# Optimization experiments

Measured on AMD Instinct MI355X. Metric: run time of the kernel, lower is better.

## Reference

```python
import jax, jax.numpy as jnp
import numpy as np

H = 128; F = 64; G = 50; L = 4; CUT = 10.0
M = 256; K = 8; A = 32
N_TOPO = M * A; N = M * K * A; NCONF = M * K
E_CONF = N * 16; E_GRAPH = N_TOPO * 4
ATOM_TYPES = 100; BOND_TYPES = 10
OFFSETS = jnp.linspace(0.0, CUT, G)
GCOEFF = -0.5 / (CUT / (G - 1)) ** 2  # GaussianSmearing coeff
BN_EPS = 1e-5


def batchnorm(x, g, b):
    # BatchNorm1d in training mode: batch statistics over nodes
    mu = x.mean(0)
    var = ((x - mu) ** 2).mean(0)
    return (x - mu) * jax.lax.rsqrt(var + BN_EPS) * g + b


def setup_inputs():
    key = jax.random.key(0)
    ks = jax.random.split(key, 20)
    s = lambda k, shp: (jax.random.normal(k, shp) * 0.05).astype(jnp.float32)
    inp = {}
    inp["x_topo"] = jax.random.randint(ks[0], (N_TOPO,), 0, ATOM_TYPES)
    inp["pos"] = jax.random.normal(ks[1], (N, 3), dtype=jnp.float32) * 3.0
    inp["edge_index_conf"] = jax.random.randint(ks[2], (2, E_CONF), 0, N)
    inp["edge_index_graph"] = jax.random.randint(ks[3], (2, E_GRAPH), 0, N_TOPO)
    inp["edge_attr_graph"] = jax.random.randint(ks[4], (E_GRAPH,), 0, BOND_TYPES)
    # conf_node_batch: for molecule i, repeat arange(A)+i*A over K conformers
    cnb = (np.arange(M)[:, None, None] * A + np.broadcast_to(np.arange(A), (K, A))).reshape(-1)
    inp["conf_node_batch"] = jnp.asarray(cnb, dtype=jnp.int32)
    inp["pos_batch"] = jnp.repeat(jnp.arange(NCONF), A).astype(jnp.int32)
    inp["conf_batch"] = jnp.repeat(jnp.arange(M), K).astype(jnp.int32)
    # parameters
    inp["atom_emb"] = s(ks[5], (ATOM_TYPES, H))
    inp["cf_lin1_w"] = s(ks[6], (L, H, F))
    inp["cf_mlp_w1"] = s(ks[7], (L, G, F)); inp["cf_mlp_b1"] = jnp.zeros((L, F), jnp.float32)
    inp["cf_mlp_w2"] = s(ks[8], (L, F, F)); inp["cf_mlp_b2"] = jnp.zeros((L, F), jnp.float32)
    inp["cf_lin2_w"] = s(ks[9], (L, F, H)); inp["cf_lin2_b"] = jnp.zeros((L, H), jnp.float32)
    inp["lin_w"] = s(ks[10], (L, H, H)); inp["lin_b"] = jnp.zeros((L, H), jnp.float32)
    inp["bond_emb"] = s(ks[11], (L, BOND_TYPES, H))
    inp["gin_w1"] = s(ks[12], (L, H, H)); inp["gin_b1"] = jnp.zeros((L, H), jnp.float32)
    inp["gin_w2"] = s(ks[13], (L, H, H)); inp["gin_b2"] = jnp.zeros((L, H), jnp.float32)
    inp["gin_bn_g"] = jnp.ones((L, H), jnp.float32); inp["gin_bn_b"] = jnp.zeros((L, H), jnp.float32)
    inp["bn_g"] = jnp.ones((L, H), jnp.float32); inp["bn_b"] = jnp.zeros((L, H), jnp.float32)
    inp["gin_eps"] = jnp.zeros((L,), jnp.float32)
    inp["out_w1"] = s(ks[14], (H, H)); inp["out_b1"] = jnp.zeros((H,), jnp.float32)
    inp["out_w2"] = s(ks[15], (H, 1)); inp["out_b2"] = jnp.zeros((1,), jnp.float32)
    return inp


def _forward(x_topo, edge_index_conf, edge_index_graph, edge_attr_graph,
             conf_node_batch, pos_batch, conf_batch,
             pos, atom_emb, cf_lin1_w, cf_mlp_w1, cf_mlp_b1, cf_mlp_w2, cf_mlp_b2,
             cf_lin2_w, cf_lin2_b, lin_w, lin_b, bond_emb,
             gin_w1, gin_b1, gin_w2, gin_b2, gin_bn_g, gin_bn_b, bn_g, bn_b,
             gin_eps, out_w1, out_b1, out_w2, out_b2):
    # AtomEncoder on topo graph, broadcast to all conformers
    x = atom_emb[x_topo][conf_node_batch]                      # [N, H]
    row, col = edge_index_conf[0], edge_index_conf[1]
    d = pos[row] - pos[col]
    ew = jnp.sqrt(jnp.sum(d * d, axis=-1) + 1e-12)             # edge_weight_conf [E_conf]
    ea = jnp.exp(GCOEFF * (ew[:, None] - OFFSETS) ** 2)        # GaussianSmearing [E_conf, G]
    cwin = 0.5 * (jnp.cos(ew * jnp.pi / CUT) + 1.0)            # SchNet cosine cutoff
    gr, gc = edge_index_graph[0], edge_index_graph[1]
    for l in range(L):
        # CFConv branch (use_conf)
        Wf = (jax.nn.relu(ea @ cf_mlp_w1[l] + cf_mlp_b1[l]) @ cf_mlp_w2[l] + cf_mlp_b2[l]) * cwin[:, None]
        h = x @ cf_lin1_w[l]                                   # lin1, no bias
        agg = jax.ops.segment_sum(h[row] * Wf, col, num_segments=N)
        h = agg @ cf_lin2_w[l] + cf_lin2_b[l]                  # lin2
        h = jax.nn.relu(h)
        h = h @ lin_w[l] + lin_b[l]
        out = x + h                                            # residual
        # GIN branch on topo graph (use_graph)
        x_agg = jax.ops.segment_max(x, conf_node_batch, num_segments=N_TOPO)
        eemb = bond_emb[l][edge_attr_graph]                    # BondEncoder
        magg = jax.ops.segment_sum(jax.nn.relu(x_agg[gr] + eemb), gc, num_segments=N_TOPO)
        hg = (1.0 + gin_eps[l]) * x_agg + magg
        hg = jax.nn.relu(batchnorm(hg @ gin_w1[l] + gin_b1[l], gin_bn_g[l], gin_bn_b[l]))
        hg = hg @ gin_w2[l] + gin_b2[l]
        hg = batchnorm(hg, bn_g[l], bn_b[l])
        out = out + hg[conf_node_batch]
        x = jax.nn.relu(out)
    x = jax.ops.segment_max(x, pos_batch, num_segments=NCONF)  # pool atoms -> conformers
    x = jax.ops.segment_max(x, conf_batch, num_segments=M)     # pool conformers -> molecules
    x = jax.nn.relu(x @ out_w1 + out_b1) @ out_w2 + out_b2     # out_layer
    return x                                                   # training mode: no clamp


def reference(x_topo, pos, edge_index_conf, edge_index_graph, edge_attr_graph,
              conf_node_batch, pos_batch, conf_batch,
              atom_emb, cf_lin1_w, cf_mlp_w1, cf_mlp_b1, cf_mlp_w2, cf_mlp_b2,
              cf_lin2_w, cf_lin2_b, lin_w, lin_b, bond_emb,
              gin_w1, gin_b1, gin_w2, gin_b2, gin_bn_g, gin_bn_b, bn_g, bn_b,
              gin_eps, out_w1, out_b1, out_w2, out_b2):
    return _forward(x_topo, edge_index_conf, edge_index_graph, edge_attr_graph,
                    conf_node_batch, pos_batch, conf_batch,
                    pos, atom_emb, cf_lin1_w, cf_mlp_w1, cf_mlp_b1, cf_mlp_w2, cf_mlp_b2,
                    cf_lin2_w, cf_lin2_b, lin_w, lin_b, bond_emb,
                    gin_w1, gin_b1, gin_w2, gin_b2, gin_bn_g, gin_bn_b, bn_g, bn_b,
                    gin_eps, out_w1, out_b1, out_w2, out_b2)
```

## Files before the change

kernel.cpp:

```cpp
#include <hip/hip_runtime.h>
#include <hip/hip_bf16.h>

#define EC 1048576
#define NN 65536
#define NT 8192
#define MM 256
#define HH 128
#define FF 64
#define GG 50
#define EG 32768

#define TBL 2048
#define TBL_SHIFT 11
#define TRANGE 14.0f

#define CAP 32
#define OVF_CAP 8192
#define NEB (NN * 64 / 256)
#define SEB (8 * (EC / 256))

constexpr float STEP = 10.0f / 49.0f;
constexpr float GC = -0.5f / (STEP * STEP);

typedef __attribute__((ext_vector_type(8))) short bf16x8;
typedef __attribute__((ext_vector_type(4))) float f32x4;

__device__ __forceinline__ ushort f2b(float v) {
    __hip_bfloat16 h = __float2bfloat16(v);
    return *(ushort*)&h;
}
__device__ __forceinline__ float b2f(ushort u) {
    return __uint_as_float(((unsigned)u) << 16);
}

__global__ __launch_bounds__(256) void setup_kernel(
    const int* __restrict__ eic, const int* __restrict__ cnb,
    const int* __restrict__ eig, const float* __restrict__ pos,
    const float* __restrict__ emb, const int* __restrict__ xtopo,
    int* __restrict__ degC, ushort* __restrict__ uu16, ushort* __restrict__ xb)
{
    int b = blockIdx.x, tid = threadIdx.x;
    if (b < EC / 256) {
        int e = b * 256 + tid;
        int r = eic[e], c = eic[EC + e];
        float dx = pos[r*3+0] - pos[c*3+0];
        float dy = pos[r*3+1] - pos[c*3+1];
        float dz = pos[r*3+2] - pos[c*3+2];
        float w = sqrtf(dx*dx + dy*dy + dz*dz + 1e-12f);
        float u = fminf(w * ((TBL - 1) / TRANGE), 2046.96875f);
        uu16[e] = (ushort)(int)(u * 32.0f);
    } else if (b < EC / 256 + EG / 256) {
        atomicAdd(&degC[eig[EG + (b - EC / 256) * 256 + tid]], 1);
    } else {
        int idx = (b - EC / 256 - EG / 256) * 256 + tid;
        int n = idx >> 4;
        int f8 = (idx & 15) << 3;
        const float* e = emb + (size_t)xtopo[cnb[n]] * HH + f8;
        float4 v0 = *(const float4*)e;
        float4 v1 = *(const float4*)(e + 4);
        ushort u[8] = {f2b(v0.x), f2b(v0.y), f2b(v0.z), f2b(v0.w),
                       f2b(v1.x), f2b(v1.y), f2b(v1.z), f2b(v1.w)};
        *(bf16x8*)(xb + ((size_t)idx << 3)) = *(const bf16x8*)u;
    }
}

__global__ __launch_bounds__(256) void scanC_kernel(
    const int* __restrict__ degC, int* __restrict__ offsC, int* __restrict__ curC)
{
    __shared__ int s[256];
    __shared__ int base;
    int tid = threadIdx.x;
    if (tid == 0) base = 0;
    __syncthreads();
    for (int c = 0; c < NT / 256; c++) {
        int v = degC[c * 256 + tid];
        s[tid] = v;
        __syncthreads();
        for (int off = 1; off < 256; off <<= 1) {
            int t = (tid >= off) ? s[tid - off] : 0;
            __syncthreads();
            s[tid] += t;
            __syncthreads();
        }
        int excl = s[tid] - v + base;
        offsC[c * 256 + tid] = excl;
        curC[c * 256 + tid] = excl;
        __syncthreads();
        if (tid == 255) base += s[255];
        __syncthreads();
    }
    if (tid == 0) offsC[NT] = EG;
}

__global__ __launch_bounds__(256) void scatter_all_kernel(
    const int* __restrict__ eic, const ushort* __restrict__ uu16,
    const int* __restrict__ eig, const int* __restrict__ eattr,
    int* __restrict__ cntA, int* __restrict__ curC,
    int* __restrict__ pay_pad, int2* __restrict__ gpay,
    int* __restrict__ ovf_cnt, int2* __restrict__ ovf)
{
    int b = blockIdx.x, tid = threadIdx.x;
    if (b < SEB) {
        int part = b & 7;
        int e = (b >> 3) * 256 + tid;
        int c = eic[EC + e];
        if ((c >> 13) != part) return;
        int pay = ((int)uu16[e] << 16) | (eic[e] & 0xFFFF);
        int slot = atomicAdd(&cntA[c], 1);
        if (slot < CAP) {
            pay_pad[c * CAP + slot] = pay;
        } else {
            int o = atomicAdd(ovf_cnt, 1);
            if (o < OVF_CAP) ovf[o] = make_int2(c, pay);
        }
    } else {
        int e = (b - SEB) * 256 + tid;
        int p = atomicAdd(&curC[eig[EG + e]], 1);
        gpay[p] = make_int2(eig[e], eattr[e]);
    }
}

__global__ __launch_bounds__(64) void build_table_kernel(
    const float* __restrict__ w1a, const float* __restrict__ b1a,
    const float* __restrict__ w2a, const float* __restrict__ b2a,
    float* __restrict__ table_all)
{
    int l = blockIdx.x >> TBL_SHIFT;
    int p = blockIdx.x & (TBL - 1);
    int lane = threadIdx.x;
    const float* w1 = w1a + (size_t)l * GG * FF;
    const float* b1 = b1a + (size_t)l * FF;
    const float* w2 = w2a + (size_t)l * FF * FF;
    const float* b2 = b2a + (size_t)l * FF;
    float w = p * (TRANGE / (TBL - 1));
    float t = b1[lane];
    for (int g = 0; g < GG; g++) {
        float d = w - g * STEP;
        float ea = __expf(GC * d * d);
        t = fmaf(ea, w1[g * 64 + lane], t);
    }
    __shared__ float ts[64];
    ts[lane] = fmaxf(t, 0.f);
    __syncthreads();
    float wf = b2[lane];
    for (int i = 0; i < 64; i++)
        wf = fmaf(ts[i], w2[i * 64 + lane], wf);
    float cw = 0.5f * (__cosf(w * (3.14159265358979323846f / 10.0f)) + 1.0f);
    table_all[((size_t)l * TBL + p) * 64 + lane] = wf * cw;
}

__global__ __launch_bounds__(256) void pack_table_kernel(
    const float* __restrict__ table_all, ushort2* __restrict__ table2_all)
{
    int idx = blockIdx.x * 256 + threadIdx.x;
    int f = idx & 63;
    int rest = idx >> 6;
    int i = rest & (TBL - 1);
    int l = rest >> TBL_SHIFT;
    const float* T = table_all + ((size_t)l * TBL) * 64;
    float t0 = T[(size_t)i * 64 + f];
    float t1 = (i + 1 < TBL) ? T[(size_t)(i + 1) * 64 + f] : 0.f;
    table2_all[idx] = make_ushort2(f2b(t0), f2b(t1 - t0));
}

__device__ __forceinline__ void prep_one(
    const float* __restrict__ W, ushort* __restrict__ Wf, int K, int N, int idx)
{
    int sz = K * N;
    int l = idx / sz;
    int t = idx - l * sz;
    int j = t & 7;
    int lane = (t >> 3) & 63;
    int rest = t >> 9;
    int KTl = K >> 5;
    int kt = rest % KTl;
    int nt = rest / KTl;
    int k = kt * 32 + (lane >> 4) * 8 + j;
    int n = nt * 16 + (lane & 15);
    Wf[idx] = f2b(W[(size_t)l * sz + (size_t)k * N + n]);
}

__global__ __launch_bounds__(256) void prep_all_kernel(
    const float* __restrict__ cf_lin1_w, const float* __restrict__ cf_lin2_w,
    const float* __restrict__ lin_w, const float* __restrict__ gin_w1,
    const float* __restrict__ gin_w2,
    ushort* __restrict__ w1f, ushort* __restrict__ w2f, ushort* __restrict__ wlf,
    ushort* __restrict__ gw1f, ushort* __restrict__ gw2f)
{
    int b = blockIdx.x, tid = threadIdx.x;
    if (b < 128)       prep_one(cf_lin1_w, w1f, HH, FF, b * 256 + tid);
    else if (b < 256)  prep_one(cf_lin2_w, w2f, FF, HH, (b - 128) * 256 + tid);
    else if (b < 512)  prep_one(lin_w, wlf, HH, HH, (b - 256) * 256 + tid);
    else if (b < 768)  prep_one(gin_w1, gw1f, HH, HH, (b - 512) * 256 + tid);
    else               prep_one(gin_w2, gw2f, HH, HH, (b - 768) * 256 + tid);
}

__global__ __launch_bounds__(256) void gemm_bf16_kernel(
    const ushort* __restrict__ A, const ushort* __restrict__ Bf,
    ushort* __restrict__ Cb)
{
    int tid = threadIdx.x;
    int wave = tid >> 6, lane = tid & 63;
    int m0 = (blockIdx.x * 4 + wave) * 16;
    int arow = m0 + (lane & 15);
    int ak = (lane >> 4) * 8;
    bf16x8 a[4];
    const ushort* Ap = A + (size_t)arow * 128 + ak;
    #pragma unroll
    for (int kt = 0; kt < 4; kt++)
        a[kt] = *(const bf16x8*)(Ap + kt * 32);
    f32x4 acc[4];
    #pragma unroll
    for (int i = 0; i < 4; i++) acc[i] = (f32x4){0.f, 0.f, 0.f, 0.f};
    const ushort* Bp = Bf + (size_t)lane * 8;
    #pragma unroll
    for (int nt = 0; nt < 4; nt++)
        #pragma unroll
        for (int kt = 0; kt < 4; kt++) {
            bf16x8 b = *(const bf16x8*)(Bp + ((size_t)(nt * 4 + kt)) * 512);
            acc[nt] = __builtin_amdgcn_mfma_f32_16x16x32_bf16(a[kt], b, acc[nt], 0, 0, 0);
        }
    int col0 = lane & 15;
    int rbase = m0 + (lane >> 4) * 4;
    #pragma unroll
    for (int nt = 0; nt < 4; nt++) {
        int col = nt * 16 + col0;
        #pragma unroll
        for (int r = 0; r < 4; r++)
            Cb[(size_t)(rbase + r) * 64 + col] = f2b(acc[nt][r]);
    }
}

#define EDGE8(BASE) { \
    int pq[8]; \
    int4 q0 = *(const int4*)(pp + BASE); \
    int4 q1 = *(const int4*)(pp + BASE + 4); \
    pq[0]=q0.x; pq[1]=q0.y; pq[2]=q0.z; pq[3]=q0.w; \
    pq[4]=q1.x; pq[5]=q1.y; pq[6]=q1.z; pq[7]=q1.w; \
    _Pragma("unroll") \
    for (int q = 0; q < 8; q++) pq[q] = (BASE + q < n1) ? pq[q] : 0; \
    float h[8]; \
    _Pragma("unroll") \
    for (int q = 0; q < 8; q++) \
        h[q] = b2f(h1b[(size_t)(pq[q] & 0xFFFF) * 64 + lane]); \
    unsigned tt[8]; \
    _Pragma("unroll") \
    for (int q = 0; q < 8; q++) \
        tt[q] = *(const unsigned*)(table2 + (size_t)((unsigned)pq[q] >> 21) * 64 + lane); \
    _Pragma("unroll") \
    for (int q = 0; q < 8; q++) { \
        float fr = (float)(((unsigned)pq[q] >> 16) & 31) * F32; \
        float t0 = __uint_as_float(tt[q] << 16); \
        float dt = __uint_as_float(tt[q] & 0xFFFF0000u); \
        float hq = (BASE + q < n1) ? h[q] : 0.f; \
        float wf = fmaf(dt, fr, t0); \
        if (q & 1) acc1 = fmaf(hq, wf, acc1); else acc0 = fmaf(hq, wf, acc0); \
    } }

__global__ __launch_bounds__(256) void edge_xagg_kernel(
    const int* __restrict__ cntA, const int* __restrict__ pay_pad,
    const int* __restrict__ ovf_cnt, const int2* __restrict__ ovf,
    const ushort2* __restrict__ table2, const ushort* __restrict__ h1b,
    ushort* __restrict__ aggb,
    const ushort* __restrict__ xb, ushort* __restrict__ xaggb)
{
    int tid = threadIdx.x;
    if (blockIdx.x < NEB) {
        int node = (blockIdx.x * 256 + tid) >> 6;
        int lane = tid & 63;
        int deg = cntA[node];
        int n1 = min(deg, CAP);
        const int* pp = pay_pad + (size_t)node * CAP;
        const float F32 = 0.03125f;
        float acc0 = 0.f, acc1 = 0.f;
        {
            int pay[16];
            int4 p0 = *(const int4*)(pp);
            int4 p1 = *(const int4*)(pp + 4);
            int4 p2 = *(const int4*)(pp + 8);
            int4 p3 = *(const int4*)(pp + 12);
            pay[0]=p0.x; pay[1]=p0.y; pay[2]=p0.z; pay[3]=p0.w;
            pay[4]=p1.x; pay[5]=p1.y; pay[6]=p1.z; pay[7]=p1.w;
            pay[8]=p2.x; pay[9]=p2.y; pay[10]=p2.z; pay[11]=p2.w;
            pay[12]=p3.x; pay[13]=p3.y; pay[14]=p3.z; pay[15]=p3.w;
            #pragma unroll
            for (int q = 0; q < 16; q++) pay[q] = (q < n1) ? pay[q] : 0;
            float h[16];
            #pragma unroll
            for (int q = 0; q < 16; q++)
                h[q] = b2f(h1b[(size_t)(pay[q] & 0xFFFF) * 64 + lane]);
            unsigned tt[16];
            #pragma unroll
            for (int q = 0; q < 16; q++)
                tt[q] = *(const unsigned*)(table2 + (size_t)((unsigned)pay[q] >> 21) * 64 + lane);
            #pragma unroll
            for (int q = 0; q < 16; q++) {
                float fr = (float)(((unsigned)pay[q] >> 16) & 31) * F32;
                float t0 = __uint_as_float(tt[q] << 16);
                float dt = __uint_as_float(tt[q] & 0xFFFF0000u);
                float hq = (q < n1) ? h[q] : 0.f;
                float wf = fmaf(dt, fr, t0);
                if (q & 1) acc1 = fmaf(hq, wf, acc1); else acc0 = fmaf(hq, wf, acc0);
            }
        }
        if (n1 > 16) {
            EDGE8(16);
            if (n1 > 24) EDGE8(24);
        }
        float acc = acc0 + acc1;
        if (deg > CAP) {
            int no = min(*ovf_cnt, OVF_CAP);
            for (int j = 0; j < no; j++) {
                int2 o = ovf[j];
                if (o.x == node) {
                    unsigned uf = (unsigned)o.y >> 16;
                    int i0 = uf >> 5;
                    float fr = (float)(uf & 31) * F32;
                    ushort2 ttv = table2[(size_t)i0 * 64 + lane];
                    acc = fmaf(b2f(h1b[(size_t)(o.y & 0xFFFF) * 64 + lane]),
                               fmaf(b2f(ttv.y), fr, b2f(ttv.x)), acc);
                }
            }
        }
        aggb[(size_t)node * 64 + lane] = f2b(acc);
    } else {
        int idx = (blockIdx.x - NEB) * 256 + tid;
        int tn = idx >> 7, f = idx & 127;
        int m = tn >> 5, a = tn & 31;
        const ushort* base = xb + ((size_t)((m << 8) + a)) * HH + f;
        float mx = -3.4e38f;
        #pragma unroll
        for (int k = 0; k < 8; k++)
            mx = fmaxf(mx, b2f(base[(size_t)(k << 5) * HH]));
        xaggb[idx] = f2b(mx);
    }
}

#define TSTR 136

__global__ __launch_bounds__(256) void gin_gemm1_kernel(
    const int* __restrict__ goffs, const int2* __restrict__ gpay,
    const ushort* __restrict__ xaggb, const float* __restrict__ bemb,
    const float* __restrict__ eps, const ushort* __restrict__ Bf,
    const float* __restrict__ bias, ushort* __restrict__ Cb,
    float* __restrict__ gsum, float* __restrict__ gsq)
{
    __shared__ ushort hg0s[64 * TSTR];
    __shared__ float ssum[128], ssq[128];
    int tid = threadIdx.x;
    if (tid < 128) { ssum[tid] = 0.f; ssq[tid] = 0.f; }
    {
        int row = tid >> 2;
        int fc = (tid & 3) * 32;
        int tn = blockIdx.x * 64 + row;
        float e1 = 1.0f + eps[0];
        float acc[32];
        const ushort* xo = xaggb + (size_t)tn * HH + fc;
        #pragma unroll
        for (int c = 0; c < 4; c++) {
            bf16x8 x = *(const bf16x8*)(xo + c * 8);
            #pragma unroll
            for (int j = 0; j < 8; j++)
                acc[c * 8 + j] = e1 * b2f((ushort)x[j]);
        }
        int beg = goffs[tn], end = goffs[tn + 1];
        for (int p = beg; p < end; p++) {
            int2 g = gpay[p];
            const ushort* xs = xaggb + (size_t)g.x * HH + fc;
            const float* bs = bemb + (size_t)g.y * HH + fc;
            #pragma unroll
            for (int c = 0; c < 4; c++) {
                bf16x8 x = *(const bf16x8*)(xs + c * 8);
                float4 b0 = *(const float4*)(bs + c * 8);
                float4 b1 = *(const float4*)(bs + c * 8 + 4);
                float bb[8] = {b0.x, b0.y, b0.z, b0.w, b1.x, b1.y, b1.z, b1.w};
                #pragma unroll
                for (int j = 0; j < 8; j++)
                    acc[c * 8 + j] += fmaxf(b2f((ushort)x[j]) + bb[j], 0.f);
            }
        }
        ushort* dst = hg0s + row * TSTR + fc;
        #pragma unroll
        for (int j = 0; j < 32; j++) dst[j] = f2b(acc[j]);
    }
    __syncthreads();
    int wave = tid >> 6, lane = tid & 63;
    int lm = lane & 15, lq = lane >> 4;
    int ak = lq * 8;
    bf16x8 a[4];
    #pragma unroll
    for (int kt = 0; kt < 4; kt++)
        a[kt] = *(const bf16x8*)&hg0s[(wave * 16 + lm) * TSTR + ak + kt * 32];
    f32x4 acc[8];
    #pragma unroll
    for (int i = 0; i < 8; i++) acc[i] = (f32x4){0.f, 0.f, 0.f, 0.f};
    const ushort* Bp = Bf + (size_t)lane * 8;
    #pragma unroll
    for (int nt = 0; nt < 8; nt++)
        #pragma unroll
        for (int kt = 0; kt < 4; kt++) {
            bf16x8 b = *(const bf16x8*)(Bp + ((size_t)(nt * 4 + kt)) * 512);
            acc[nt] = __builtin_amdgcn_mfma_f32_16x16x32_bf16(a[kt], b, acc[nt], 0, 0, 0);
        }
    int rbase = blockIdx.x * 64 + wave * 16 + lq * 4;
    #pragma unroll
    for (int nt = 0; nt < 8; nt++) {
        int col = nt * 16 + lm;
        float bs = bias[col];
        float ps = 0.f, pq = 0.f;
        #pragma unroll
        for (int r = 0; r < 4; r++) {
            float v = acc[nt][r] + bs;
            Cb[(size_t)(rbase + r) * 128 + col] = f2b(v);
            ps += v; pq += v * v;
        }
        atomicAdd(&ssum[col], ps);
        atomicAdd(&ssq[col], pq);
    }
    __syncthreads();
    if (tid < 128) {
        atomicAdd(&gsum[tid], ssum[tid]);
        atomicAdd(&gsq[tid], ssq[tid]);
    }
}

__global__ __launch_bounds__(256) void gemm_bn_stats_kernel(
    const ushort* __restrict__ Araw, const float* __restrict__ sum1,
    const float* __restrict__ sq1, const float* __restrict__ g1,
    const float* __restrict__ bb1, const ushort* __restrict__ Bf,
    const float* __restrict__ bias, ushort* __restrict__ Cb,
    float* __restrict__ gsum, float* __restrict__ gsq)
{
    __shared__ float ssum[128], ssq[128];
    int tid = threadIdx.x;
    if (tid < 128) { ssum[tid] = 0.f; ssq[tid] = 0.f; }
    __syncthreads();
    int wave = tid >> 6, lane = tid & 63;
    int m0 = (blockIdx.x * 4 + wave) * 16;
    int arow = m0 + (lane & 15);
    int ak = (lane >> 4) * 8;
    const float INV_NT = 1.0f / NT;
    bf16x8 a[4];
    const ushort* Ap = Araw + (size_t)arow * 128 + ak;
    #pragma unroll
    for (int kt = 0; kt < 4; kt++) {
        bf16x8 raw = *(const bf16x8*)(Ap + kt * 32);
        ushort ub[8];
        #pragma unroll
        for (int j = 0; j < 8; j++) {
            int k = ak + kt * 32 + j;
            float mu = sum1[k] * INV_NT;
            float var = sq1[k] * INV_NT - mu * mu;
            float inv = rsqrtf(var + 1e-5f);
            float w = fmaxf((b2f((ushort)raw[j]) - mu) * inv * g1[k] + bb1[k], 0.f);
            ub[j] = f2b(w);
        }
        a[kt] = *(bf16x8*)ub;
    }
    f32x4 acc[8];
    #pragma unroll
    for (int i = 0; i < 8; i++) acc[i] = (f32x4){0.f, 0.f, 0.f, 0.f};
    const ushort* Bp = Bf + (size_t)lane * 8;
    #pragma unroll
    for (int nt = 0; nt < 8; nt++)
        #pragma unroll
        for (int kt = 0; kt < 4; kt++) {
            bf16x8 b = *(const bf16x8*)(Bp + ((size_t)(nt * 4 + kt)) * 512);
            acc[nt] = __builtin_amdgcn_mfma_f32_16x16x32_bf16(a[kt], b, acc[nt], 0, 0, 0);
        }
    int col0 = lane & 15;
    int rbase = m0 + (lane >> 4) * 4;
    #pragma unroll
    for (int nt = 0; nt < 8; nt++) {
        int col = nt * 16 + col0;
        float bs = bias[col];
        float ps = 0.f, pq = 0.f;
        #pragma unroll
        for (int r = 0; r < 4; r++) {
            float v = acc[nt][r] + bs;
            Cb[(size_t)(rbase + r) * 128 + col] = f2b(v);
            ps += v; pq += v * v;
        }
        atomicAdd(&ssum[col], ps);
        atomicAdd(&ssq[col], pq);
    }
    __syncthreads();
    if (tid < 128) {
        atomicAdd(&gsum[tid], ssum[tid]);
        atomicAdd(&gsq[tid], ssq[tid]);
    }
}

__global__ __launch_bounds__(256) void fused_lin_kernel(
    const ushort* __restrict__ aggb, const ushort* __restrict__ w2,
    const float* __restrict__ b2, const ushort* __restrict__ w3,
    const float* __restrict__ b3, const ushort* __restrict__ hgBb,
    const float* __restrict__ sum2, const float* __restrict__ sq2,
    const float* __restrict__ g2, const float* __restrict__ bb2,
    const int* __restrict__ cnb, const ushort* __restrict__ w1n,
    ushort* __restrict__ xb, ushort* __restrict__ h1b)
{
    __shared__ ushort t1s[4][16 * TSTR];
    __shared__ ushort t2s[4][16 * TSTR];
    int tid = threadIdx.x;
    int wave = tid >> 6, lane = tid & 63;
    int m0 = (blockIdx.x * 4 + wave) * 16;
    int lm = lane & 15;
    int lq = lane >> 4;
    ushort* T1 = t1s[wave];
    ushort* T2 = t2s[wave];
    const float INV_NT = 1.0f / NT;

    const ushort* Ap = aggb + (size_t)(m0 + lm) * 64 + lq * 8;
    bf16x8 a1[2];
    a1[0] = *(const bf16x8*)(Ap);
    a1[1] = *(const bf16x8*)(Ap + 32);
    f32x4 acc[8];
    #pragma unroll
    for (int i = 0; i < 8; i++) acc[i] = (f32x4){0.f, 0.f, 0.f, 0.f};
    {
        const ushort* Bp = w2 + (size_t)lane * 8;
        #pragma unroll
        for (int nt = 0; nt < 8; nt++)
            #pragma unroll
            for (int kt = 0; kt < 2; kt++) {
                bf16x8 b = *(const bf16x8*)(Bp + ((size_t)(nt * 2 + kt)) * 512);
                acc[nt] = __builtin_amdgcn_mfma_f32_16x16x32_bf16(a1[kt], b, acc[nt], 0, 0, 0);
            }
    }
    #pragma unroll
    for (int nt = 0; nt < 8; nt++) {
        int col = nt * 16 + lm;
        float bs = b2[col];
        #pragma unroll
        for (int r = 0; r < 4; r++) {
            float v = fmaxf(acc[nt][r] + bs, 0.f);
            T1[(lq * 4 + r) * TSTR + col] = f2b(v);
        }
    }
    __syncthreads();

    bf16x8 a2[4];
    #pragma unroll
    for (int kt = 0; kt < 4; kt++)
        a2[kt] = *(const bf16x8*)&T1[lm * TSTR + kt * 32 + lq * 8];
    __syncthreads();
    #pragma unroll
    for (int i = 0; i < 4; i++) {
        int idx = i * 64 + lane;
        int row = idx >> 4, ch = idx & 15;
        bf16x8 v = *(const bf16x8*)(xb + (size_t)(m0 + row) * HH + ch * 8);
        *(bf16x8*)&T1[row * TSTR + ch * 8] = v;
    }
    #pragma unroll
    for (int i = 0; i < 8; i++) acc[i] = (f32x4){0.f, 0.f, 0.f, 0.f};
    {
        const ushort* Bp = w3 + (size_t)lane * 8;
        #pragma unroll
        for (int nt = 0; nt < 8; nt++)
            #pragma unroll
            for (int kt = 0; kt < 4; kt++) {
                bf16x8 b = *(const bf16x8*)(Bp + ((size_t)(nt * 4 + kt)) * 512);
                acc[nt] = __builtin_amdgcn_mfma_f32_16x16x32_bf16(a2[kt], b, acc[nt], 0, 0, 0);
            }
    }
    int rbase = m0 + lq * 4;
    int cn[4];
    #pragma unroll
    for (int r = 0; r < 4; r++) cn[r] = cnb[rbase + r];
    #pragma unroll
    for (int nt = 0; nt < 8; nt++) {
        int col = nt * 16 + lm;
        float bs = b3[col];
        float mu2 = sum2[col] * INV_NT;
        float var2 = sq2[col] * INV_NT - mu2 * mu2;
        float sc2 = rsqrtf(var2 + 1e-5f) * g2[col];
        float sh2 = bb2[col] - mu2 * sc2;
        #pragma unroll
        for (int r = 0; r < 4; r++) {
            float v = acc[nt][r] + bs;
            v += b2f(T1[(lq * 4 + r) * TSTR + col]);
            v = fmaf(b2f(hgBb[(size_t)cn[r] * HH + col]), sc2, v + sh2);
            v = fmaxf(v, 0.f);
            T2[(lq * 4 + r) * TSTR + col] = f2b(v);
        }
    }
    __syncthreads();
    #pragma unroll
    for (int i = 0; i < 4; i++) {
        int idx = i * 64 + lane;
        int row = idx >> 4, ch = idx & 15;
        bf16x8 v = *(const bf16x8*)&T2[row * TSTR + ch * 8];
        *(bf16x8*)(xb + (size_t)(m0 + row) * HH + ch * 8) = v;
    }
    if (!w1n) return;
    __syncthreads();

    bf16x8 a3[4];
    #pragma unroll
    for (int kt = 0; kt < 4; kt++)
        a3[kt] = *(const bf16x8*)&T2[lm * TSTR + kt * 32 + lq * 8];
    f32x4 acc3[4];
    #pragma unroll
    for (int i = 0; i < 4; i++) acc3[i] = (f32x4){0.f, 0.f, 0.f, 0.f};
    {
        const ushort* Bp = w1n + (size_t)lane * 8;
        #pragma unroll
        for (int nt = 0; nt < 4; nt++)
            #pragma unroll
            for (int kt = 0; kt < 4; kt++) {
                bf16x8 b = *(const bf16x8*)(Bp + ((size_t)(nt * 4 + kt)) * 512);
                acc3[nt] = __builtin_amdgcn_mfma_f32_16x16x32_bf16(a3[kt], b, acc3[nt], 0, 0, 0);
            }
    }
    #pragma unroll
    for (int nt = 0; nt < 4; nt++) {
        int col = nt * 16 + lm;
        #pragma unroll
        for (int r = 0; r < 4; r++)
            T1[(lq * 4 + r) * TSTR + col] = f2b(acc3[nt][r]);
    }
    __syncthreads();
    #pragma unroll
    for (int i = 0; i < 2; i++) {
        int idx = i * 64 + lane;
        int row = idx >> 3, ch = idx & 7;
        bf16x8 v = *(const bf16x8*)&T1[row * TSTR + ch * 8];
        *(bf16x8*)(h1b + (size_t)(m0 + row) * FF + ch * 8) = v;
    }
}

__global__ __launch_bounds__(128) void out_layer_kernel(
    const ushort* __restrict__ xb, const float* __restrict__ w1,
    const float* __restrict__ b1, const float* __restrict__ w2,
    const float* __restrict__ b2, float* __restrict__ out)
{
    int m = blockIdx.x, f = threadIdx.x;
    const ushort* base = xb + (size_t)m * 256 * HH + f;
    float mx = -3.4e38f;
    for (int r = 0; r < 256; r++)
        mx = fmaxf(mx, b2f(base[(size_t)r * HH]));
    __shared__ float xs[128];
    xs[f] = mx;
    __syncthreads();
    float acc = b1[f];
    for (int k = 0; k < 128; k++) acc = fmaf(xs[k], w1[k * HH + f], acc);
    acc = fmaxf(acc, 0.f) * w2[f];
    __shared__ float red[128];
    red[f] = acc;
    __syncthreads();
    for (int off = 64; off > 0; off >>= 1) {
        if (f < off) red[f] += red[f + off];
        __syncthreads();
    }
    if (f == 0) out[m] = red[0] + b2[0];
}

extern "C" void kernel_launch(void* const* d_in, const int* in_sizes, int n_in,
                              void* d_out, int out_size, void* d_ws, size_t ws_size,
                              hipStream_t stream)
{
    const int*   x_topo    = (const int*)d_in[0];
    const float* pos       = (const float*)d_in[1];
    const int*   eic       = (const int*)d_in[2];
    const int*   eig       = (const int*)d_in[3];
    const int*   eattr     = (const int*)d_in[4];
    const int*   cnb       = (const int*)d_in[5];
    const float* atom_emb  = (const float*)d_in[8];
    const float* cf_lin1_w = (const float*)d_in[9];
    const float* cf_mlp_w1 = (const float*)d_in[10];
    const float* cf_mlp_b1 = (const float*)d_in[11];
    const float* cf_mlp_w2 = (const float*)d_in[12];
    const float* cf_mlp_b2 = (const float*)d_in[13];
    const float* cf_lin2_w = (const float*)d_in[14];
    const float* cf_lin2_b = (const float*)d_in[15];
    const float* lin_w     = (const float*)d_in[16];
    const float* lin_b     = (const float*)d_in[17];
    const float* bond_emb  = (const float*)d_in[18];
    const float* gin_w1    = (const float*)d_in[19];
    const float* gin_b1    = (const float*)d_in[20];
    const float* gin_w2    = (const float*)d_in[21];
    const float* gin_b2    = (const float*)d_in[22];
    const float* gin_bn_g  = (const float*)d_in[23];
    const float* gin_bn_b  = (const float*)d_in[24];
    const float* bn_g      = (const float*)d_in[25];
    const float* bn_b      = (const float*)d_in[26];
    const float* gin_eps   = (const float*)d_in[27];
    const float* out_w1    = (const float*)d_in[28];
    const float* out_b1    = (const float*)d_in[29];
    const float* out_w2    = (const float*)d_in[30];
    const float* out_b2    = (const float*)d_in[31];
    float* out = (float*)d_out;

    char* wsb = (char*)d_ws;
    size_t off = 0;
    auto alloc = [&](size_t nbytes) -> void* {
        void* p = (void*)(wsb + off);
        off += (nbytes + 255) & ~(size_t)255;
        return p;
    };
    ushort* uu16    = (ushort*)alloc(EC * 2);
    ushort* xb      = (ushort*)alloc((size_t)NN * HH * 2);
    ushort* h1b     = (ushort*)alloc((size_t)NN * FF * 2);
    ushort* aggb    = (ushort*)alloc((size_t)NN * FF * 2);
    ushort* xaggb   = (ushort*)alloc((size_t)NT * HH * 2);
    ushort* hgA     = (ushort*)alloc((size_t)NT * HH * 2);
    ushort* hgB     = (ushort*)alloc((size_t)NT * HH * 2);
    float*  table_all  = (float*)alloc((size_t)4 * TBL * 64 * 4);
    ushort2* table2_all = (ushort2*)alloc((size_t)4 * TBL * 64 * 4);
    float*  stats   = (float*)alloc((size_t)4 * 4 * 128 * 4);
    int*    cntA    = (int*)alloc((size_t)NN * 4);
    int*    degC    = (int*)alloc((size_t)NT * 4);
    int*    ovf_cnt = (int*)alloc(256);
    int*    offsC   = (int*)alloc((NT + 1) * 4);
    int*    curC    = (int*)alloc(NT * 4);
    int*    pay_pad = (int*)alloc((size_t)NN * CAP * 4);
    int2*   ovf     = (int2*)alloc((size_t)OVF_CAP * 8);
    int2*   gpay    = (int2*)alloc((size_t)EG * 8);
    ushort* w1f     = (ushort*)alloc((size_t)4 * HH * FF * 2);
    ushort* w2f     = (ushort*)alloc((size_t)4 * FF * HH * 2);
    ushort* wlf     = (ushort*)alloc((size_t)4 * HH * HH * 2);
    ushort* gw1f    = (ushort*)alloc((size_t)4 * HH * HH * 2);
    ushort* gw2f    = (ushort*)alloc((size_t)4 * HH * HH * 2);

    hipMemsetAsync(stats, 0,
        ((size_t)4 * 4 * 128 * 4 + 255 & ~(size_t)255) +
        ((size_t)NN * 4 + 255 & ~(size_t)255) +
        ((size_t)NT * 4 + 255 & ~(size_t)255) + 256, stream);

    setup_kernel<<<EC / 256 + EG / 256 + NN * HH / 8 / 256, 256, 0, stream>>>(
        eic, cnb, eig, pos, atom_emb, x_topo, degC, uu16, xb);
    scanC_kernel<<<1, 256, 0, stream>>>(degC, offsC, curC);
    scatter_all_kernel<<<SEB + EG / 256, 256, 0, stream>>>(
        eic, uu16, eig, eattr, cntA, curC, pay_pad, gpay, ovf_cnt, ovf);

    build_table_kernel<<<4 * TBL, 64, 0, stream>>>(
        cf_mlp_w1, cf_mlp_b1, cf_mlp_w2, cf_mlp_b2, table_all);
    pack_table_kernel<<<4 * TBL * 64 / 256, 256, 0, stream>>>(table_all, table2_all);
    prep_all_kernel<<<1024, 256, 0, stream>>>(
        cf_lin1_w, cf_lin2_w, lin_w, gin_w1, gin_w2, w1f, w2f, wlf, gw1f, gw2f);

    gemm_bf16_kernel<<<NN / 64, 256, 0, stream>>>(xb, w1f, h1b);

    for (int l = 0; l < 4; l++) {
        const ushort2* table2 = table2_all + (size_t)l * TBL * 64;
        float* sum1 = stats + (size_t)l * 512;
        float* sq1  = sum1 + 128;
        float* sum2 = sum1 + 256;
        float* sq2  = sum1 + 384;
        edge_xagg_kernel<<<NEB + NT * HH / 256, 256, 0, stream>>>(
            cntA, pay_pad, ovf_cnt, ovf, table2, h1b, aggb, xb, xaggb);
        gin_gemm1_kernel<<<NT / 64, 256, 0, stream>>>(
            offsC, gpay, xaggb, bond_emb + (size_t)l * 10 * HH, gin_eps + l,
            gw1f + (size_t)l * HH * HH, gin_b1 + (size_t)l * HH, hgA, sum1, sq1);
        gemm_bn_stats_kernel<<<NT / 64, 256, 0, stream>>>(
            hgA, sum1, sq1, gin_bn_g + (size_t)l * HH, gin_bn_b + (size_t)l * HH,
            gw2f + (size_t)l * HH * HH, gin_b2 + (size_t)l * HH, hgB, sum2, sq2);
        fused_lin_kernel<<<NN / 64, 256, 0, stream>>>(
            aggb, w2f + (size_t)l * FF * HH, cf_lin2_b + (size_t)l * HH,
            wlf + (size_t)l * HH * HH, lin_b + (size_t)l * HH,
            hgB, sum2, sq2, bn_g + (size_t)l * HH, bn_b + (size_t)l * HH,
            cnb, (l < 3) ? (w1f + (size_t)(l + 1) * HH * FF) : nullptr,
            xb, h1b);
    }

    out_layer_kernel<<<MM, 128, 0, stream>>>(xb, out_w1, out_b1, out_w2, out_b2, out);
}
```

Measured before the change: 695.3 us.

## Pre-fill edge payload slots with zero-table sentinel and make edge loop uniform

Fills the padded per-node edge payload array with a sentinel that points at a zeroed last table row, so unused slots contribute nothing without per-slot masking. The edge aggregation loop then runs in uniform 8-edge chunks gated by degree, with payloads broadcast through readfirstlane and byte-offset address math. The 1/32 fraction scale is folded into the packed table delta. This costs an extra memset-style pass over the payload buffer in setup and relies on the last table row being unused by real edges.

```diff
diff --git a/kernel.cpp b/kernel.cpp
--- a/kernel.cpp
+++ b/kernel.cpp
@@ -19,6 +19,8 @@
 #define NEB (NN * 64 / 256)
 #define SEB (8 * (EC / 256))
 
+#define SENT 0xFFE00000
+
 constexpr float STEP = 10.0f / 49.0f;
 constexpr float GC = -0.5f / (STEP * STEP);
 
@@ -33,14 +35,19 @@
     return __uint_as_float(((unsigned)u) << 16);
 }
 
+#define SETUP_B0 (EC / 256)
+#define SETUP_B1 (SETUP_B0 + EG / 256)
+#define SETUP_B2 (SETUP_B1 + NN * HH / 8 / 256)
+#define SETUP_B3 (SETUP_B2 + NN * CAP / 4 / 256)
 __global__ __launch_bounds__(256) void setup_kernel(
     const int* __restrict__ eic, const int* __restrict__ cnb,
     const int* __restrict__ eig, const float* __restrict__ pos,
     const float* __restrict__ emb, const int* __restrict__ xtopo,
-    int* __restrict__ degC, ushort* __restrict__ uu16, ushort* __restrict__ xb)
+    int* __restrict__ degC, ushort* __restrict__ uu16, ushort* __restrict__ xb,
+    int4* __restrict__ pay_pad4)
 {
     int b = blockIdx.x, tid = threadIdx.x;
-    if (b < EC / 256) {
+    if (b < SETUP_B0) {
         int e = b * 256 + tid;
         int r = eic[e], c = eic[EC + e];
         float dx = pos[r*3+0] - pos[c*3+0];
@@ -49,10 +56,10 @@
         float w = sqrtf(dx*dx + dy*dy + dz*dz + 1e-12f);
         float u = fminf(w * ((TBL - 1) / TRANGE), 2046.96875f);
         uu16[e] = (ushort)(int)(u * 32.0f);
-    } else if (b < EC / 256 + EG / 256) {
-        atomicAdd(&degC[eig[EG + (b - EC / 256) * 256 + tid]], 1);
-    } else {
-        int idx = (b - EC / 256 - EG / 256) * 256 + tid;
+    } else if (b < SETUP_B1) {
+        atomicAdd(&degC[eig[EG + (b - SETUP_B0) * 256 + tid]], 1);
+    } else if (b < SETUP_B2) {
+        int idx = (b - SETUP_B1) * 256 + tid;
         int n = idx >> 4;
         int f8 = (idx & 15) << 3;
         const float* e = emb + (size_t)xtopo[cnb[n]] * HH + f8;
@@ -61,6 +68,9 @@
         ushort u[8] = {f2b(v0.x), f2b(v0.y), f2b(v0.z), f2b(v0.w),
                        f2b(v1.x), f2b(v1.y), f2b(v1.z), f2b(v1.w)};
         *(bf16x8*)(xb + ((size_t)idx << 3)) = *(const bf16x8*)u;
+    } else {
+        int idx = (b - SETUP_B2) * 256 + tid;
+        pay_pad4[idx] = make_int4(SENT, SENT, SENT, SENT);
     }
 }
 
@@ -157,10 +167,14 @@
     int rest = idx >> 6;
     int i = rest & (TBL - 1);
     int l = rest >> TBL_SHIFT;
+    if (i == TBL - 1) {
+        table2_all[idx] = make_ushort2(0, 0);
+        return;
+    }
     const float* T = table_all + ((size_t)l * TBL) * 64;
     float t0 = T[(size_t)i * 64 + f];
-    float t1 = (i + 1 < TBL) ? T[(size_t)(i + 1) * 64 + f] : 0.f;
-    table2_all[idx] = make_ushort2(f2b(t0), f2b(t1 - t0));
+    float t1 = T[(size_t)(i + 1) * 64 + f];
+    table2_all[idx] = make_ushort2(f2b(t0), f2b((t1 - t0) * 0.03125f));
 }
 
 __device__ __forceinline__ void prep_one(
@@ -233,28 +247,31 @@
 
 #define EDGE8(BASE) { \
     int pq[8]; \
-    int4 q0 = *(const int4*)(pp + BASE); \
-    int4 q1 = *(const int4*)(pp + BASE + 4); \
-    pq[0]=q0.x; pq[1]=q0.y; pq[2]=q0.z; pq[3]=q0.w; \
-    pq[4]=q1.x; pq[5]=q1.y; pq[6]=q1.z; pq[7]=q1.w; \
-    _Pragma("unroll") \
-    for (int q = 0; q < 8; q++) pq[q] = (BASE + q < n1) ? pq[q] : 0; \
+    { int4 q0 = *(const int4*)(pp + BASE); \
+      int4 q1 = *(const int4*)(pp + BASE + 4); \
+      pq[0]=__builtin_amdgcn_readfirstlane(q0.x); \
+      pq[1]=__builtin_amdgcn_readfirstlane(q0.y); \
+      pq[2]=__builtin_amdgcn_readfirstlane(q0.z); \
+      pq[3]=__builtin_amdgcn_readfirstlane(q0.w); \
+      pq[4]=__builtin_amdgcn_readfirstlane(q1.x); \
+      pq[5]=__builtin_amdgcn_readfirstlane(q1.y); \
+      pq[6]=__builtin_amdgcn_readfirstlane(q1.z); \
+      pq[7]=__builtin_amdgcn_readfirstlane(q1.w); } \
     float h[8]; \
     _Pragma("unroll") \
     for (int q = 0; q < 8; q++) \
-        h[q] = b2f(h1b[(size_t)(pq[q] & 0xFFFF) * 64 + lane]); \
+        h[q] = b2f(*(const ushort*)(h1c + ((((unsigned)(pq[q] & 0xFFFF)) << 7) + lane2))); \
     unsigned tt[8]; \
     _Pragma("unroll") \
     for (int q = 0; q < 8; q++) \
-        tt[q] = *(const unsigned*)(table2 + (size_t)((unsigned)pq[q] >> 21) * 64 + lane); \
+        tt[q] = *(const unsigned*)(tbc + (((((unsigned)pq[q]) >> 21) << 8) + lane4)); \
     _Pragma("unroll") \
     for (int q = 0; q < 8; q++) { \
-        float fr = (float)(((unsigned)pq[q] >> 16) & 31) * F32; \
+        float fr = (float)((unsigned)((pq[q] >> 16) & 31)); \
         float t0 = __uint_as_float(tt[q] << 16); \
-        float dt = __uint_as_float(tt[q] & 0xFFFF0000u); \
-        float hq = (BASE + q < n1) ? h[q] : 0.f; \
-        float wf = fmaf(dt, fr, t0); \
-        if (q & 1) acc1 = fmaf(hq, wf, acc1); else acc0 = fmaf(hq, wf, acc0); \
+        float dts = __uint_as_float(tt[q] & 0xFFFF0000u); \
+        float wf = fmaf(dts, fr, t0); \
+        if (q & 1) acc1 = fmaf(h[q], wf, acc1); else acc0 = fmaf(h[q], wf, acc0); \
     } }
 
 __global__ __launch_bounds__(256) void edge_xagg_kernel(
@@ -266,46 +283,23 @@
 {
     int tid = threadIdx.x;
     if (blockIdx.x < NEB) {
-        int node = (blockIdx.x * 256 + tid) >> 6;
         int lane = tid & 63;
+        int node = __builtin_amdgcn_readfirstlane((blockIdx.x * 256 + tid) >> 6);
+        unsigned lane2 = (unsigned)lane * 2;
+        unsigned lane4 = (unsigned)lane * 4;
+        const char* h1c = (const char*)h1b;
+        const char* tbc = (const char*)table2;
         int deg = cntA[node];
         int n1 = min(deg, CAP);
         const int* pp = pay_pad + (size_t)node * CAP;
-        const float F32 = 0.03125f;
         float acc0 = 0.f, acc1 = 0.f;
-        {
-            int pay[16];
-            int4 p0 = *(const int4*)(pp);
-            int4 p1 = *(const int4*)(pp + 4);
-            int4 p2 = *(const int4*)(pp + 8);
-            int4 p3 = *(const int4*)(pp + 12);
-            pay[0]=p0.x; pay[1]=p0.y; pay[2]=p0.z; pay[3]=p0.w;
-            pay[4]=p1.x; pay[5]=p1.y; pay[6]=p1.z; pay[7]=p1.w;
-            pay[8]=p2.x; pay[9]=p2.y; pay[10]=p2.z; pay[11]=p2.w;
-            pay[12]=p3.x; pay[13]=p3.y; pay[14]=p3.z; pay[15]=p3.w;
-            #pragma unroll
-            for (int q = 0; q < 16; q++) pay[q] = (q < n1) ? pay[q] : 0;
-            float h[16];
-            #pragma unroll
-            for (int q = 0; q < 16; q++)
-                h[q] = b2f(h1b[(size_t)(pay[q] & 0xFFFF) * 64 + lane]);
-            unsigned tt[16];
-            #pragma unroll
-            for (int q = 0; q < 16; q++)
-                tt[q] = *(const unsigned*)(table2 + (size_t)((unsigned)pay[q] >> 21) * 64 + lane);
-            #pragma unroll
-            for (int q = 0; q < 16; q++) {
-                float fr = (float)(((unsigned)pay[q] >> 16) & 31) * F32;
-                float t0 = __uint_as_float(tt[q] << 16);
-                float dt = __uint_as_float(tt[q] & 0xFFFF0000u);
-                float hq = (q < n1) ? h[q] : 0.f;
-                float wf = fmaf(dt, fr, t0);
-                if (q & 1) acc1 = fmaf(hq, wf, acc1); else acc0 = fmaf(hq, wf, acc0);
+        EDGE8(0);
+        if (n1 > 8) {
+            EDGE8(8);
+            if (n1 > 16) {
+                EDGE8(16);
+                if (n1 > 24) EDGE8(24);
             }
-        }
-        if (n1 > 16) {
-            EDGE8(16);
-            if (n1 > 24) EDGE8(24);
         }
         float acc = acc0 + acc1;
         if (deg > CAP) {
@@ -315,7 +309,7 @@
                 if (o.x == node) {
                     unsigned uf = (unsigned)o.y >> 16;
                     int i0 = uf >> 5;
-                    float fr = (float)(uf & 31) * F32;
+                    float fr = (float)(uf & 31);
                     ushort2 ttv = table2[(size_t)i0 * 64 + lane];
                     acc = fmaf(b2f(h1b[(size_t)(o.y & 0xFFFF) * 64 + lane]),
                                fmaf(b2f(ttv.y), fr, b2f(ttv.x)), acc);
@@ -728,8 +722,8 @@
         ((size_t)NN * 4 + 255 & ~(size_t)255) +
         ((size_t)NT * 4 + 255 & ~(size_t)255) + 256, stream);
 
-    setup_kernel<<<EC / 256 + EG / 256 + NN * HH / 8 / 256, 256, 0, stream>>>(
-        eic, cnb, eig, pos, atom_emb, x_topo, degC, uu16, xb);
+    setup_kernel<<<SETUP_B3, 256, 0, stream>>>(
+        eic, cnb, eig, pos, atom_emb, x_topo, degC, uu16, xb, (int4*)pay_pad);
     scanC_kernel<<<1, 256, 0, stream>>>(degC, offsC, curC);
     scatter_all_kernel<<<SEB + EG / 256, 256, 0, stream>>>(
         eic, uu16, eig, eattr, cntA, curC, pay_pad, gpay, ovf_cnt, ovf);
```

Result: faster. 632.3 us (-9.1%).
